# Optimization experiments

Hardware: AMD Instinct MI355X
Metric: run time of the kernel (lower is better)

Reference implementation:

```python
import jax, jax.numpy as jnp
import numpy as np

N = 4096      # num nodes
D = 256       # hidden_dim
H = 4         # num attention heads (separate single-head MHA modules)
E = 131072    # num edges
EPS = 1e-5


def setup_inputs() -> dict:
    key = jax.random.key(0)
    ks = jax.random.split(key, 12)
    s = 0.02
    x = jax.random.normal(ks[0], (N, D), dtype=jnp.float32)
    edge_index = jax.random.randint(ks[1], (2, E), 0, N, dtype=jnp.int64)
    # per-head in_proj split into q/k/v, stacked over heads [H, D, D]
    Wq = jax.random.normal(ks[2], (H, D, D), dtype=jnp.float32) * s
    Wk = jax.random.normal(ks[3], (H, D, D), dtype=jnp.float32) * s
    Wv = jax.random.normal(ks[4], (H, D, D), dtype=jnp.float32) * s
    bq = jnp.zeros((H, D), dtype=jnp.float32)
    bk = jnp.zeros((H, D), dtype=jnp.float32)
    bv = jnp.zeros((H, D), dtype=jnp.float32)
    Wo = jax.random.normal(ks[5], (H, D, D), dtype=jnp.float32) * s  # per-head MHA out_proj
    bo = jnp.zeros((H, D), dtype=jnp.float32)
    Wp = jax.random.normal(ks[6], (D, H * D), dtype=jnp.float32) * s  # output_projection
    bp = jnp.zeros((D,), dtype=jnp.float32)
    gamma = jnp.ones((D,), dtype=jnp.float32)
    beta = jnp.zeros((D,), dtype=jnp.float32)
    return dict(x=x, edge_index=edge_index, Wq=Wq, bq=bq, Wk=Wk, bk=bk,
                Wv=Wv, bv=bv, Wo=Wo, bo=bo, Wp=Wp, bp=bp, gamma=gamma, beta=beta)


def _build_mask(edge_index, n):
    row, col = edge_index[0], edge_index[1]
    mask = jnp.full((n, n), -jnp.inf, dtype=jnp.float32)
    mask = mask.at[row, col].set(0.0)
    mask = mask.at[col, row].set(0.0)
    mask = mask.at[jnp.arange(n), jnp.arange(n)].set(0.0)
    return mask


def reference(x, edge_index, Wq, bq, Wk, bk, Wv, bv, Wo, bo, Wp, bp, gamma, beta):
    mask = _build_mask(edge_index, x.shape[0])  # [N, N] additive, -inf on non-edges
    # per-head projections (torch Linear: x @ W.T + b); h = head axis
    q = jnp.einsum('nd,hed->hne', x, Wq) + bq[:, None, :]
    k = jnp.einsum('nd,hed->hne', x, Wk) + bk[:, None, :]
    v = jnp.einsum('nd,hed->hne', x, Wv) + bv[:, None, :]
    scores = jnp.einsum('hne,hme->hnm', q, k) / jnp.sqrt(jnp.float32(D)) + mask[None]
    attn = jax.nn.softmax(scores, axis=-1)                    # [H, N, N]
    o = jnp.einsum('hnm,hme->hne', attn, v)                   # [H, N, D]
    head_out = jnp.einsum('hne,hfe->hnf', o, Wo) + bo[:, None, :]  # per-head out_proj
    concatenated = jnp.transpose(head_out, (1, 0, 2)).reshape(x.shape[0], H * D)
    out = concatenated @ Wp.T + bp                             # [N, D]
    mu = jnp.mean(out, axis=-1, keepdims=True)
    var = jnp.mean(jnp.square(out - mu), axis=-1, keepdims=True)
    return (out - mu) / jnp.sqrt(var + EPS) * gamma + beta
```

## Files before the change

### kernel.cpp

```cpp
#include <hip/hip_runtime.h>
#include <hip/hip_bf16.h>

#define N_NODES 4096
#define DIM 256
#define NHEAD 4
#define NEDGE 131072
#define MWORDS 128
#define MAXDEG 192
#define GBK 64

typedef unsigned short ushort_t;
typedef __attribute__((ext_vector_type(8))) short short8;
typedef __attribute__((ext_vector_type(4))) float f32x4;

__device__ __forceinline__ ushort_t f2bf(float f) {
    unsigned u = __float_as_uint(f);
    unsigned r = u + 0x7FFFu + ((u >> 16) & 1u);
    return (ushort_t)(r >> 16);
}
__device__ __forceinline__ float bf2f(ushort_t u) {
    return __uint_as_float((unsigned)u << 16);
}

__global__ __launch_bounds__(256) void build_mask_kernel(const int* __restrict__ ei,
                                                         unsigned* __restrict__ mask) {
    const int t = blockIdx.x * blockDim.x + threadIdx.x;
    if (t < NEDGE) {
        const int r = ei[t] & (N_NODES - 1);
        const int c = ei[NEDGE + t] & (N_NODES - 1);
        atomicOr(&mask[r * MWORDS + (c >> 5)], 1u << (c & 31));
        atomicOr(&mask[c * MWORDS + (r >> 5)], 1u << (r & 31));
    } else if (t < NEDGE + N_NODES) {
        const int i = t - NEDGE;
        atomicOr(&mask[i * MWORDS + (i >> 5)], 1u << (i & 31));
    }
}

__global__ __launch_bounds__(256) void convert_all_kernel(
    const float* __restrict__ x,  const float* __restrict__ Wq,
    const float* __restrict__ Wk, const float* __restrict__ Wv,
    const float* __restrict__ Wo, const float* __restrict__ Wp,
    ushort_t* __restrict__ xb, ushort_t* __restrict__ wstack,
    ushort_t* __restrict__ wob, ushort_t* __restrict__ wpb) {
    const int e = (blockIdx.x * blockDim.x + threadIdx.x) << 2;
    const float* src; ushort_t* dst; int off;
    if (e < 1048576)      { src = x;  dst = xb;              off = e; }
    else if (e < 1310720) { src = Wq; dst = wstack;          off = e - 1048576; }
    else if (e < 1572864) { src = Wk; dst = wstack + 262144; off = e - 1310720; }
    else if (e < 1835008) { src = Wv; dst = wstack + 524288; off = e - 1572864; }
    else if (e < 2097152) { src = Wo; dst = wob;             off = e - 1835008; }
    else                  { src = Wp; dst = wpb;             off = e - 2097152; }
    const float4 v = *(const float4*)(src + off);
    ushort4 r;
    r.x = f2bf(v.x); r.y = f2bf(v.y); r.z = f2bf(v.z); r.w = f2bf(v.w);
    *(ushort4*)(dst + off) = r;
}

template <int MODE>
__global__ __launch_bounds__(256) void mfma_gemm_kernel(
    const ushort_t* __restrict__ Wb, const ushort_t* __restrict__ Xb,
    const float* __restrict__ b0, const float* __restrict__ b1,
    const float* __restrict__ b2,
    ushort_t* __restrict__ qb, ushort_t* __restrict__ kvh,
    void* __restrict__ outp, int K) {
    __shared__ ushort_t Wt[128][GBK + 8];
    __shared__ ushort_t Xt[128][GBK + 8];
    const int tid = threadIdx.x;
    const int lane = tid & 63;
    const int wid = tid >> 6;
    const int wr = wid >> 1, wc = wid & 1;
    const int zoff = (MODE == 1) ? blockIdx.z : 0;
    const ushort_t* Wp_ = Wb + (size_t)zoff * (256 * 256);
    const ushort_t* Xp_ = Xb + (size_t)zoff * ((size_t)N_NODES * 256);
    const int chB = blockIdx.x * 128;
    const int ndB = blockIdx.y * 128;

    f32x4 acc[4][4] = {};

    for (int kt = 0; kt < K; kt += GBK) {
        short8 wreg[4], xreg[4];
#pragma unroll
        for (int i = 0; i < 4; ++i) {
            const int flat = tid + (i << 8);
            const int r = flat >> 3, s = flat & 7;
            wreg[i] = *(const short8*)(Wp_ + (size_t)(chB + r) * K + kt + (s << 3));
            xreg[i] = *(const short8*)(Xp_ + (size_t)(ndB + r) * K + kt + (s << 3));
        }
        __syncthreads();
#pragma unroll
        for (int i = 0; i < 4; ++i) {
            const int flat = tid + (i << 8);
            const int r = flat >> 3, s = flat & 7;
            *(short8*)&Wt[r][s << 3] = wreg[i];
            *(short8*)&Xt[r][s << 3] = xreg[i];
        }
        __syncthreads();
#pragma unroll
        for (int kk = 0; kk < 2; ++kk) {
            short8 af[4], bf[4];
            const int ko = (kk << 5) + ((lane >> 4) << 3);
#pragma unroll
            for (int m = 0; m < 4; ++m)
                af[m] = *(const short8*)&Wt[wr * 64 + m * 16 + (lane & 15)][ko];
#pragma unroll
            for (int n = 0; n < 4; ++n)
                bf[n] = *(const short8*)&Xt[wc * 64 + n * 16 + (lane & 15)][ko];
#pragma unroll
            for (int m = 0; m < 4; ++m)
#pragma unroll
                for (int n = 0; n < 4; ++n)
                    acc[m][n] = __builtin_amdgcn_mfma_f32_16x16x32_bf16(
                        af[m], bf[n], acc[m][n], 0, 0, 0);
        }
    }

    const int lhi = lane >> 4;
    const int llo = lane & 15;
    int op = 0, h = 0;
    if (MODE == 0) { op = chB >> 10; h = (chB >> 8) & 3; }
#pragma unroll
    for (int m = 0; m < 4; ++m) {
        const int ch = chB + wr * 64 + m * 16 + (lhi << 2);
        float4 bia;
        if (MODE == 0) {
            const float* bb = (op == 0 ? b0 : op == 1 ? b1 : b2) + (h << 8);
            bia = *(const float4*)&bb[ch & 255];
        } else if (MODE == 1) {
            bia = *(const float4*)&b0[(zoff << 8) + ch];
        } else {
            bia = *(const float4*)&b0[ch];
        }
#pragma unroll
        for (int n = 0; n < 4; ++n) {
            const int node = ndB + wc * 64 + n * 16 + llo;
            const float v0 = acc[m][n][0] + bia.x;
            const float v1 = acc[m][n][1] + bia.y;
            const float v2 = acc[m][n][2] + bia.z;
            const float v3 = acc[m][n][3] + bia.w;
            if (MODE == 2) {
                float4 r; r.x = v0; r.y = v1; r.z = v2; r.w = v3;
                *(float4*)&((float*)outp)[((size_t)node << 8) + ch] = r;
            } else {
                ushort4 r;
                r.x = f2bf(v0); r.y = f2bf(v1); r.z = f2bf(v2); r.w = f2bf(v3);
                if (MODE == 1) {
                    *(ushort4*)&((ushort_t*)outp)[(size_t)node * 1024 + (zoff << 8) + ch] = r;
                } else {
                    const int c = ch & 255;
                    if (op == 0)
                        *(ushort4*)&qb[(((size_t)h * N_NODES + node) << 8) + c] = r;
                    else if (op == 1)
                        *(ushort4*)&kvh[(((size_t)h * N_NODES + node) << 9) + c] = r;
                    else
                        *(ushort4*)&kvh[(((size_t)h * N_NODES + node) << 9) + 256 + c] = r;
                }
            }
        }
    }
}

__global__ __launch_bounds__(256) void attn_sparse_kernel(const unsigned* __restrict__ mask,
                                                          const ushort_t* __restrict__ qb,
                                                          const ushort_t* __restrict__ kvh,
                                                          ushort_t* __restrict__ ob) {
    __shared__ int nbr[4][MAXDEG];
    __shared__ int cnt[4];
    const int tid = threadIdx.x;
    const int w = tid >> 6;
    const int lane = tid & 63;
    const int xcd = blockIdx.x & 7;
    const int h = xcd >> 1;
    const int node = ((xcd & 1) << 11) + ((blockIdx.x >> 3) << 2) + w;

    if (lane == 0) cnt[w] = 0;
    __syncthreads();
    for (int t = lane; t < MWORDS; t += 64) {
        unsigned m = mask[node * MWORDS + t];
        while (m) {
            const int b = __ffs(m) - 1;
            m &= m - 1;
            const int pos = atomicAdd(&cnt[w], 1);
            if (pos < MAXDEG) nbr[w][pos] = (t << 5) + b;
        }
    }
    __syncthreads();
    const int deg = cnt[w] < MAXDEG ? cnt[w] : MAXDEG;

    const ushort4 qu = *(const ushort4*)&qb[(((size_t)h * N_NODES + node) << 8) + (lane << 2)];
    const float qx = bf2f(qu.x), qy = bf2f(qu.y), qz = bf2f(qu.z), qw = bf2f(qu.w);
    const ushort_t* base = kvh + ((size_t)h * N_NODES << 9) + (lane << 2);

    const float SC = 0.0625f * 1.44269504f;
    float denom = 0.f;
    float4 oa = {0.f, 0.f, 0.f, 0.f};

    for (int n = 0; n < deg; ++n) {
        const int j = nbr[w][n];
        const ushort_t* kp = base + ((size_t)j << 9);
        const ushort4 ku = *(const ushort4*)kp;
        const ushort4 vu = *(const ushort4*)(kp + 256);
        float p = qx * bf2f(ku.x) + qy * bf2f(ku.y)
                + qz * bf2f(ku.z) + qw * bf2f(ku.w);
        p += __shfl_xor(p, 1);
        p += __shfl_xor(p, 2);
        p += __shfl_xor(p, 4);
        p += __shfl_xor(p, 8);
        p += __shfl_xor(p, 16);
        p += __shfl_xor(p, 32);
        const float wt = __builtin_amdgcn_exp2f(p * SC);
        denom += wt;
        oa.x += wt * bf2f(vu.x);
        oa.y += wt * bf2f(vu.y);
        oa.z += wt * bf2f(vu.z);
        oa.w += wt * bf2f(vu.w);
    }
    const float inv = 1.0f / denom;
    ushort4 r;
    r.x = f2bf(oa.x * inv); r.y = f2bf(oa.y * inv);
    r.z = f2bf(oa.z * inv); r.w = f2bf(oa.w * inv);
    *(ushort4*)&ob[(((size_t)h * N_NODES + node) << 8) + (lane << 2)] = r;
}

__global__ __launch_bounds__(256) void layernorm_kernel(const float* __restrict__ inp,
                                                        const float* __restrict__ gamma,
                                                        const float* __restrict__ beta,
                                                        float* __restrict__ out) {
    const int row = (blockIdx.x << 2) + (threadIdx.x >> 6);
    const int lane = threadIdx.x & 63;
    const float4 xv = *(const float4*)&inp[row * DIM + (lane << 2)];
    float s = xv.x + xv.y + xv.z + xv.w;
#pragma unroll
    for (int off = 32; off; off >>= 1) s += __shfl_xor(s, off);
    const float mu = s * (1.0f / DIM);
    const float dx = xv.x - mu, dy = xv.y - mu, dz = xv.z - mu, dw = xv.w - mu;
    float sq = dx * dx + dy * dy + dz * dz + dw * dw;
#pragma unroll
    for (int off = 32; off; off >>= 1) sq += __shfl_xor(sq, off);
    const float inv = 1.0f / sqrtf(sq * (1.0f / DIM) + 1e-5f);
    const float4 gv = *(const float4*)&gamma[lane << 2];
    const float4 bv = *(const float4*)&beta[lane << 2];
    float4 r;
    r.x = dx * inv * gv.x + bv.x;
    r.y = dy * inv * gv.y + bv.y;
    r.z = dz * inv * gv.z + bv.z;
    r.w = dw * inv * gv.w + bv.w;
    *(float4*)&out[row * DIM + (lane << 2)] = r;
}

extern "C" void kernel_launch(void* const* d_in, const int* in_sizes, int n_in,
                              void* d_out, int out_size, void* d_ws, size_t ws_size,
                              hipStream_t stream) {
    const float* x     = (const float*)d_in[0];
    const int*   ei    = (const int*)d_in[1];
    const float* Wq    = (const float*)d_in[2];
    const float* bq    = (const float*)d_in[3];
    const float* Wk    = (const float*)d_in[4];
    const float* bk    = (const float*)d_in[5];
    const float* Wv    = (const float*)d_in[6];
    const float* bv    = (const float*)d_in[7];
    const float* Wo    = (const float*)d_in[8];
    const float* bo    = (const float*)d_in[9];
    const float* Wp    = (const float*)d_in[10];
    const float* bp    = (const float*)d_in[11];
    const float* gamma = (const float*)d_in[12];
    const float* beta  = (const float*)d_in[13];
    float* outf = (float*)d_out;

    char* ws = (char*)d_ws;
    unsigned* mask    = (unsigned*)(ws);
    ushort_t* xb      = (ushort_t*)(ws + (size_t)( 2 << 20));
    ushort_t* qb      = (ushort_t*)(ws + (size_t)( 4 << 20));
    ushort_t* kvh     = (ushort_t*)(ws + (size_t)(12 << 20));
    ushort_t* ob      = (ushort_t*)(ws + (size_t)(28 << 20));
    ushort_t* concatb = (ushort_t*)(ws + (size_t)(36 << 20));
    float*    outp    = (float*)  (ws + (size_t)(44 << 20));
    ushort_t* wstack  = (ushort_t*)(ws + (size_t)(48 << 20));
    ushort_t* wob     = (ushort_t*)(ws + (size_t)(50 << 20));
    ushort_t* wpb     = (ushort_t*)(ws + (size_t)(51 << 20));

    hipMemsetAsync(mask, 0, N_NODES * MWORDS * sizeof(unsigned), stream);
    build_mask_kernel<<<(NEDGE + N_NODES + 255) / 256, 256, 0, stream>>>(ei, mask);

    convert_all_kernel<<<2304, 256, 0, stream>>>(x, Wq, Wk, Wv, Wo, Wp,
                                                 xb, wstack, wob, wpb);

    mfma_gemm_kernel<0><<<dim3(24, 32), 256, 0, stream>>>(
        wstack, xb, bq, bk, bv, qb, kvh, nullptr, 256);

    attn_sparse_kernel<<<N_NODES, 256, 0, stream>>>(mask, qb, kvh, ob);

    mfma_gemm_kernel<1><<<dim3(2, 32, NHEAD), 256, 0, stream>>>(
        wob, ob, bo, nullptr, nullptr, nullptr, nullptr, concatb, 256);

    mfma_gemm_kernel<2><<<dim3(2, 32), 256, 0, stream>>>(
        wpb, concatb, bp, nullptr, nullptr, nullptr, nullptr, outp, 1024);

    layernorm_kernel<<<N_NODES / 4, 256, 0, stream>>>(outp, gamma, beta, outf);
}
```

Before: 248.3 us.

## Process four neighbors per wave in sparse attention and build lists via prefix scan

The sparse attention kernel now splits each wave into four 16-lane groups, each handling a different neighbor with 16 bf16 elements per lane. Each group uses wider 16-byte loads, and the dot-product reduction needs fewer shuffles. Partial sums are combined across groups at the end. Neighbor list construction replaces the shared-memory atomic counter with a wave-level popcount prefix scan, which removes contention on the atomic. In exchange, each lane holds more registers (16 q values and 16 accumulators), and the final cross-group reduction adds extra shuffles.

After: 201.7 us. -18.7%, faster.

```diff
diff --git a/kernel.cpp b/kernel.cpp
--- a/kernel.cpp
+++ b/kernel.cpp
@@ -164,7 +164,6 @@
                                                           const ushort_t* __restrict__ kvh,
                                                           ushort_t* __restrict__ ob) {
     __shared__ int nbr[4][MAXDEG];
-    __shared__ int cnt[4];
     const int tid = threadIdx.x;
     const int w = tid >> 6;
     const int lane = tid & 63;
@@ -172,53 +171,97 @@
     const int h = xcd >> 1;
     const int node = ((xcd & 1) << 11) + ((blockIdx.x >> 3) << 2) + w;
 
-    if (lane == 0) cnt[w] = 0;
+    const unsigned m0 = mask[node * MWORDS + lane];
+    const unsigned m1 = mask[node * MWORDS + 64 + lane];
+    const int c = __popc(m0) + __popc(m1);
+    int s = c;
+#pragma unroll
+    for (int d = 1; d < 64; d <<= 1) {
+        const int t = __shfl_up(s, d);
+        if (lane >= d) s += t;
+    }
+    const int deg0 = __shfl(s, 63);
+    const int deg = deg0 < MAXDEG ? deg0 : MAXDEG;
+    int pos = s - c;
+    unsigned mm = m0;
+    int bj = lane << 5;
+    while (mm) {
+        const int b = __ffs(mm) - 1; mm &= mm - 1;
+        if (pos < MAXDEG) nbr[w][pos] = bj + b;
+        ++pos;
+    }
+    mm = m1; bj = (lane + 64) << 5;
+    while (mm) {
+        const int b = __ffs(mm) - 1; mm &= mm - 1;
+        if (pos < MAXDEG) nbr[w][pos] = bj + b;
+        ++pos;
+    }
     __syncthreads();
-    for (int t = lane; t < MWORDS; t += 64) {
-        unsigned m = mask[node * MWORDS + t];
-        while (m) {
-            const int b = __ffs(m) - 1;
-            m &= m - 1;
-            const int pos = atomicAdd(&cnt[w], 1);
-            if (pos < MAXDEG) nbr[w][pos] = (t << 5) + b;
-        }
-    }
-    __syncthreads();
-    const int deg = cnt[w] < MAXDEG ? cnt[w] : MAXDEG;
-
-    const ushort4 qu = *(const ushort4*)&qb[(((size_t)h * N_NODES + node) << 8) + (lane << 2)];
-    const float qx = bf2f(qu.x), qy = bf2f(qu.y), qz = bf2f(qu.z), qw = bf2f(qu.w);
-    const ushort_t* base = kvh + ((size_t)h * N_NODES << 9) + (lane << 2);
-
+
+    const int sub = lane >> 4;
+    const int sl = lane & 15;
+
+    const ushort_t* qp = qb + (((size_t)h * N_NODES + node) << 8) + (sl << 4);
+    const short8 q0 = *(const short8*)qp;
+    const short8 q1 = *(const short8*)(qp + 8);
+    float qf[16];
+#pragma unroll
+    for (int i = 0; i < 8; ++i) {
+        qf[i] = bf2f((ushort_t)q0[i]);
+        qf[8 + i] = bf2f((ushort_t)q1[i]);
+    }
+    float oa[16];
+#pragma unroll
+    for (int i = 0; i < 16; ++i) oa[i] = 0.f;
+    float denom = 0.f;
+
+    const ushort_t* kbase = kvh + (((size_t)h * N_NODES) << 9) + (sl << 4);
     const float SC = 0.0625f * 1.44269504f;
-    float denom = 0.f;
-    float4 oa = {0.f, 0.f, 0.f, 0.f};
-
-    for (int n = 0; n < deg; ++n) {
-        const int j = nbr[w][n];
-        const ushort_t* kp = base + ((size_t)j << 9);
-        const ushort4 ku = *(const ushort4*)kp;
-        const ushort4 vu = *(const ushort4*)(kp + 256);
-        float p = qx * bf2f(ku.x) + qy * bf2f(ku.y)
-                + qz * bf2f(ku.z) + qw * bf2f(ku.w);
+
+    for (int n0 = 0; n0 < deg; n0 += 4) {
+        const int idx = n0 + sub;
+        const bool valid = idx < deg;
+        const int j = nbr[w][valid ? idx : 0];
+        const ushort_t* kp = kbase + ((size_t)j << 9);
+        const short8 k0 = *(const short8*)kp;
+        const short8 k1 = *(const short8*)(kp + 8);
+        const short8 v0 = *(const short8*)(kp + 256);
+        const short8 v1 = *(const short8*)(kp + 264);
+        float p = 0.f;
+#pragma unroll
+        for (int i = 0; i < 8; ++i)
+            p += qf[i] * bf2f((ushort_t)k0[i]) + qf[8 + i] * bf2f((ushort_t)k1[i]);
         p += __shfl_xor(p, 1);
         p += __shfl_xor(p, 2);
         p += __shfl_xor(p, 4);
         p += __shfl_xor(p, 8);
-        p += __shfl_xor(p, 16);
-        p += __shfl_xor(p, 32);
-        const float wt = __builtin_amdgcn_exp2f(p * SC);
+        const float wt = valid ? __builtin_amdgcn_exp2f(p * SC) : 0.f;
         denom += wt;
-        oa.x += wt * bf2f(vu.x);
-        oa.y += wt * bf2f(vu.y);
-        oa.z += wt * bf2f(vu.z);
-        oa.w += wt * bf2f(vu.w);
-    }
-    const float inv = 1.0f / denom;
-    ushort4 r;
-    r.x = f2bf(oa.x * inv); r.y = f2bf(oa.y * inv);
-    r.z = f2bf(oa.z * inv); r.w = f2bf(oa.w * inv);
-    *(ushort4*)&ob[(((size_t)h * N_NODES + node) << 8) + (lane << 2)] = r;
+#pragma unroll
+        for (int i = 0; i < 8; ++i) {
+            oa[i] += wt * bf2f((ushort_t)v0[i]);
+            oa[8 + i] += wt * bf2f((ushort_t)v1[i]);
+        }
+    }
+    denom += __shfl_xor(denom, 16);
+    denom += __shfl_xor(denom, 32);
+#pragma unroll
+    for (int i = 0; i < 16; ++i) {
+        oa[i] += __shfl_xor(oa[i], 16);
+        oa[i] += __shfl_xor(oa[i], 32);
+    }
+    if (sub == 0) {
+        const float inv = 1.0f / denom;
+        short8 r0, r1;
+#pragma unroll
+        for (int i = 0; i < 8; ++i) {
+            r0[i] = (short)f2bf(oa[i] * inv);
+            r1[i] = (short)f2bf(oa[8 + i] * inv);
+        }
+        ushort_t* op_ = ob + (((size_t)h * N_NODES + node) << 8) + (sl << 4);
+        *(short8*)op_ = r0;
+        *(short8*)(op_ + 8) = r1;
+    }
 }
 
 __global__ __launch_bounds__(256) void layernorm_kernel(const float* __restrict__ inp,
```
